# Kernel optimization log

Measured on AMD Instinct MI355X. Metric: run time of the kernel, lower is better.

The kernel has to match this reference:

```python
import jax, jax.numpy as jnp
import numpy as np

# dims: B batch, S src len, D input_size, H rnn hidden, E embedding_dim,
# V = output_size + 2 (vocab + Start/End), T = max target len (+2 for Start/End)
B, S, D, H, E, V, T = 128, 512, 256, 512, 256, 1002, 34
END = V - 1  # 'End' token index


def _gru_layer(x, h0, Wih, Whh, bih, bhh):
    """PyTorch-convention GRU layer. x: [B,T,Din], h0: [B,H].
    Wih: [3H,Din], Whh: [3H,H]. Returns (outputs [B,T,H], h_T [B,H])."""
    def step(h, xt):
        gi = xt @ Wih.T + bih            # [B,3H]
        gh = h @ Whh.T + bhh             # [B,3H]
        i_r, i_z, i_n = jnp.split(gi, 3, axis=-1)
        h_r, h_z, h_n = jnp.split(gh, 3, axis=-1)
        r = jax.nn.sigmoid(i_r + h_r)
        z = jax.nn.sigmoid(i_z + h_z)
        n = jnp.tanh(i_n + r * h_n)
        h_new = (1.0 - z) * n + z * h
        return h_new, h_new
    hT, ys = jax.lax.scan(step, h0, jnp.swapaxes(x, 0, 1))
    return jnp.swapaxes(ys, 0, 1), hT


def _gru_stack(x, h0s, layers):
    """h0s: [L,B,H]; layers: list of (Wih,Whh,bih,bhh). Returns (out, h [L,B,H])."""
    hs = []
    y = x
    for l, (Wih, Whh, bih, bhh) in enumerate(layers):
        y, hT = _gru_layer(y, h0s[l], Wih, Whh, bih, bhh)
        hs.append(hT)
    return y, jnp.stack(hs, axis=0)


def setup_inputs() -> dict:
    key = jax.random.key(0)
    ks = jax.random.split(key, 32)
    sc = 0.05
    inp = {}
    inp['source'] = jax.random.normal(ks[0], (B, S, D), dtype=jnp.float32)
    inp['target_ids'] = jax.random.randint(ks[1], (B, T), 0, V)
    inp['lengths'] = jax.random.randint(ks[2], (B,), 2, T + 1)
    inp['emb'] = sc * jax.random.normal(ks[3], (V, E), dtype=jnp.float32)
    # encoder layer 0 (in=D) and layer 1 (in=H)
    inp['enc_Wih0'] = sc * jax.random.normal(ks[4], (3 * H, D), dtype=jnp.float32)
    inp['enc_Whh0'] = sc * jax.random.normal(ks[5], (3 * H, H), dtype=jnp.float32)
    inp['enc_bih0'] = jnp.zeros((3 * H,), jnp.float32)
    inp['enc_bhh0'] = jnp.zeros((3 * H,), jnp.float32)
    inp['enc_Wih1'] = sc * jax.random.normal(ks[6], (3 * H, H), dtype=jnp.float32)
    inp['enc_Whh1'] = sc * jax.random.normal(ks[7], (3 * H, H), dtype=jnp.float32)
    inp['enc_bih1'] = jnp.zeros((3 * H,), jnp.float32)
    inp['enc_bhh1'] = jnp.zeros((3 * H,), jnp.float32)
    # decoder layer 0 (in=E) and layer 1 (in=H)
    inp['dec_Wih0'] = sc * jax.random.normal(ks[8], (3 * H, E), dtype=jnp.float32)
    inp['dec_Whh0'] = sc * jax.random.normal(ks[9], (3 * H, H), dtype=jnp.float32)
    inp['dec_bih0'] = jnp.zeros((3 * H,), jnp.float32)
    inp['dec_bhh0'] = jnp.zeros((3 * H,), jnp.float32)
    inp['dec_Wih1'] = sc * jax.random.normal(ks[10], (3 * H, H), dtype=jnp.float32)
    inp['dec_Whh1'] = sc * jax.random.normal(ks[11], (3 * H, H), dtype=jnp.float32)
    inp['dec_bih1'] = jnp.zeros((3 * H,), jnp.float32)
    inp['dec_bhh1'] = jnp.zeros((3 * H,), jnp.float32)
    # fc: H -> 5H -> 2H -> V
    inp['fc_W1'] = sc * jax.random.normal(ks[12], (5 * H, H), dtype=jnp.float32)
    inp['fc_b1'] = jnp.zeros((5 * H,), jnp.float32)
    inp['fc_W2'] = sc * jax.random.normal(ks[13], (2 * H, 5 * H), dtype=jnp.float32)
    inp['fc_b2'] = jnp.zeros((2 * H,), jnp.float32)
    inp['fc_W3'] = sc * jax.random.normal(ks[14], (V, 2 * H), dtype=jnp.float32)
    inp['fc_b3'] = jnp.zeros((V,), jnp.float32)
    return inp


def reference(source, target_ids, lengths, emb,
              enc_Wih0, enc_Whh0, enc_bih0, enc_bhh0,
              enc_Wih1, enc_Whh1, enc_bih1, enc_bhh1,
              dec_Wih0, dec_Whh0, dec_bih0, dec_bhh0,
              dec_Wih1, dec_Whh1, dec_bih1, dec_bhh1,
              fc_W1, fc_b1, fc_W2, fc_b2, fc_W3, fc_b3):
    Bx = source.shape[0]
    h0 = jnp.zeros((2, Bx, H), source.dtype)
    # encoder: only final hidden state h [L,B,H] is used
    _, h = _gru_stack(source, h0,
                      [(enc_Wih0, enc_Whh0, enc_bih0, enc_bhh0),
                       (enc_Wih1, enc_Whh1, enc_bih1, enc_bhh1)])
    # decoder over embedded (Start + target + End + pad) sequences
    tg = emb[target_ids]                               # [B,T,E]
    out, _ = _gru_stack(tg, h,
                        [(dec_Wih0, dec_Whh0, dec_bih0, dec_bhh0),
                         (dec_Wih1, dec_Whh1, dec_bih1, dec_bhh1)])
    # pad_packed_sequence zeroes timesteps >= length; sum over time
    mask = (jnp.arange(T)[None, :] < lengths[:, None]).astype(out.dtype)  # [B,T]
    pooled = jnp.einsum('bth,bt->bh', out, mask)       # [B,H]
    x = pooled @ fc_W1.T + fc_b1
    x = x @ fc_W2.T + fc_b2
    x = x @ fc_W3.T + fc_b3
    scores = jax.nn.sigmoid(x)                         # [B,V]
    # CrossEntropyLoss against the 'End' index for every row
    logp = jax.nn.log_softmax(scores, axis=-1)
    loss = -jnp.mean(logp[:, END])
    return loss
```

## Files before the change

### kernel.cpp

```cpp
#include <hip/hip_runtime.h>
#include <hip/hip_bf16.h>
#include <math.h>

#define B_ 128
#define S_ 512
#define D_ 256
#define H_ 512
#define E_ 256
#define V_ 1002
#define T_ 34
#define END_ 1001
#define NWG_TOTAL 128
#define BH (B_ * H_)
#define GPITCH 20

typedef __attribute__((ext_vector_type(8))) short short8;
typedef __attribute__((ext_vector_type(4))) float f32x4;
typedef __attribute__((ext_vector_type(4))) int i32x4;
typedef unsigned long long u64;

__device__ __forceinline__ float bf2f(unsigned short u){
  union { unsigned int i; float f; } x; x.i = ((unsigned int)u) << 16; return x.f;
}
__device__ __forceinline__ unsigned short f2bf(float f){
  union { float f; unsigned int i; } x; x.f = f;
  unsigned int r = x.i + 0x7fffu + ((x.i >> 16) & 1u);
  return (unsigned short)(r >> 16);
}
__device__ __forceinline__ float sigm(float x){ return 1.0f / (1.0f + expf(-x)); }

__device__ __forceinline__ void store_coh8(unsigned short* p, u64 v){
  __hip_atomic_store((u64*)p, v, __ATOMIC_RELAXED, __HIP_MEMORY_SCOPE_AGENT);
}

__device__ __forceinline__ i32x4 load_flags16(const unsigned* p){
  i32x4 r;
  asm volatile("global_load_dwordx4 %0, %1, off sc0 sc1\n\ts_waitcnt vmcnt(0)"
               : "=v"(r) : "v"(p) : "memory");
  return r;
}


__global__ void f2bf_kernel(const float* __restrict__ in, unsigned short* __restrict__ out, int n){
  int i = blockIdx.x * blockDim.x + threadIdx.x;
  int stride = gridDim.x * blockDim.x;
  for (; i < n; i += stride) out[i] = f2bf(in[i]);
}

__global__ void embed_kernel(const float* __restrict__ emb, const int* __restrict__ ids,
                             unsigned short* __restrict__ out){
  int i = blockIdx.x * blockDim.x + threadIdx.x;
  if (i >= B_ * T_ * E_) return;
  int bt = i >> 8;
  int e  = i & (E_ - 1);
  out[i] = f2bf(emb[(size_t)ids[bt] * E_ + e]);
}

__global__ void build_wcat(const float* __restrict__ Wih, const float* __restrict__ Whh,
                           unsigned short* __restrict__ Wcat, int Din){
  int K = Din + H_;
  int total = 2048 * K;
  int i = blockIdx.x * blockDim.x + threadIdx.x;
  int stride = gridDim.x * blockDim.x;
  for (; i < total; i += stride){
    int n = i / K, k = i - n * K;
    int g = n >> 9, j = n & 511;
    float v;
    if (g < 2){
      int r = (g << 9) + j;
      v = (k < Din) ? Wih[(size_t)r * Din + k] : Whh[(size_t)r * H_ + (k - Din)];
    } else if (g == 2){
      v = (k < Din) ? Wih[(size_t)(1024 + j) * Din + k] : 0.0f;
    } else {
      v = (k < Din) ? 0.0f : Whh[(size_t)(1024 + j) * H_ + (k - Din)];
    }
    Wcat[i] = f2bf(v);
  }
}

__global__ void build_bias(const float* __restrict__ bih, const float* __restrict__ bhh,
                           float* __restrict__ out){
  int j = blockIdx.x * blockDim.x + threadIdx.x;
  if (j >= 512) return;
  out[j]        = bih[j] + bhh[j];
  out[512 + j]  = bih[512 + j] + bhh[512 + j];
  out[1024 + j] = bih[1024 + j];
  out[1536 + j] = bhh[1024 + j];
}


template<int KT, int XKT>
__device__ __forceinline__ void run_layer(
    float* gbuf,
    const unsigned short* __restrict__ Wc, const float* __restrict__ bias4,
    const unsigned short* __restrict__ Xbase, int x_rs, int x_ts,
    const unsigned short* __restrict__ Hread,
    unsigned short* Hwrite,
    int T, unsigned round0,
    unsigned* own_flags, int slot,
    unsigned* prod_flags, unsigned prod0,
    u64* hprev,
    int jtile, int mh, int wv, int lane)
{
  constexpr int K   = KT * 32;
  constexpr int NSL = KT / 4;
  constexpr int XQ  = XKT / 4;
  constexpr int HQ  = NSL - XQ;
  const int tid  = threadIdx.x;
  const int ln   = lane & 15;
  const int lk8  = (lane >> 4) << 3;
  const int base_m = mh * 64;

  short8 wreg[4][NSL];
  #pragma unroll
  for (int g = 0; g < 4; ++g)
    #pragma unroll
    for (int j = 0; j < NSL; ++j)
      wreg[g][j] = *reinterpret_cast<const short8*>(
          Wc + (size_t)(g * 512 + jtile * 16 + ln) * K + (size_t)(wv + 4 * j) * 32 + lk8);

  const int erow  = tid >> 2;
  const int ecol0 = (tid & 3) << 2;
  const int ej    = (jtile << 4) + ecol0;
  const int egr   = base_m + erow;
  f32x4 bR, bZ, bNI, bNH;
  #pragma unroll
  for (int c = 0; c < 4; ++c){
    bR[c]  = bias4[ej + c];
    bZ[c]  = bias4[512 + ej + c];
    bNI[c] = bias4[1024 + ej + c];
    bNH[c] = bias4[1536 + ej + c];
  }

  const unsigned* pofs = own_flags + (lane & 7) * 4;
  const unsigned* ppfs = prod_flags ? (prod_flags + (lane & 7) * 4) : nullptr;

  for (int t = 0; t < T; ++t){
    const unsigned short* Xt  = Xbase + (size_t)t * x_ts;
    const unsigned short* Hin = Hread + (size_t)t * BH;

    if (ppfs){
      const unsigned prod_t = prod0 + (unsigned)t + 1u;
      for (;;){
        i32x4 g = load_flags16(ppfs);
        bool ok = (unsigned)g.x >= prod_t && (unsigned)g.y >= prod_t &&
                  (unsigned)g.z >= prod_t && (unsigned)g.w >= prod_t;
        if (__all(ok)) break;
        __builtin_amdgcn_s_sleep(1);
      }
      __builtin_amdgcn_sched_barrier(0);
    }

    i32x4 xf[XQ][4], hf[HQ][4];
    #pragma unroll
    for (int j = 0; j < XQ; ++j){
      const int kt = wv + 4 * j;
      #pragma unroll
      for (int mt = 0; mt < 4; ++mt){
        const unsigned short* p = Xt + (size_t)(base_m + mt * 16 + ln) * x_rs + kt * 32 + lk8;
        asm volatile("global_load_dwordx4 %0, %1, off" : "=v"(xf[j][mt]) : "v"(p));
      }
    }

    {
      const unsigned own_t = round0 + (unsigned)t;
      for (;;){
        i32x4 f = load_flags16(pofs);
        bool ok = (unsigned)f.x >= own_t && (unsigned)f.y >= own_t &&
                  (unsigned)f.z >= own_t && (unsigned)f.w >= own_t;
        if (__all(ok)) break;
        __builtin_amdgcn_s_sleep(1);
      }
      __builtin_amdgcn_sched_barrier(0);
    }

    #pragma unroll
    for (int j = 0; j < HQ; ++j){
      const int kt = wv + 4 * (XQ + j);
      #pragma unroll
      for (int mt = 0; mt < 4; ++mt){
        const unsigned short* p = Hin + (size_t)(base_m + mt * 16 + ln) * H_ + (kt - XKT) * 32 + lk8;
        asm volatile("global_load_dwordx4 %0, %1, off" : "=v"(hf[j][mt]) : "v"(p));
      }
    }
    __builtin_amdgcn_sched_barrier(0);

    f32x4 acc[4][4];
    #pragma unroll
    for (int g = 0; g < 4; ++g)
      #pragma unroll
      for (int mt = 0; mt < 4; ++mt) acc[g][mt] = (f32x4){0.f, 0.f, 0.f, 0.f};

    #pragma unroll
    for (int j = 0; j < XQ; ++j)
      #pragma unroll
      for (int g = 0; g < 4; ++g)
        #pragma unroll
        for (int mt = 0; mt < 4; ++mt)
          acc[g][mt] = __builtin_amdgcn_mfma_f32_16x16x32_bf16(
              __builtin_bit_cast(short8, xf[j][mt]), wreg[g][j], acc[g][mt], 0, 0, 0);

    asm volatile("s_waitcnt vmcnt(0)" ::: "memory");
    __builtin_amdgcn_sched_barrier(0);
    #pragma unroll
    for (int j = 0; j < HQ; ++j)
      #pragma unroll
      for (int g = 0; g < 4; ++g)
        #pragma unroll
        for (int mt = 0; mt < 4; ++mt)
          acc[g][mt] = __builtin_amdgcn_mfma_f32_16x16x32_bf16(
              __builtin_bit_cast(short8, hf[j][mt]), wreg[g][XQ + j], acc[g][mt], 0, 0, 0);

    #pragma unroll
    for (int g = 0; g < 4; ++g)
      #pragma unroll
      for (int mt = 0; mt < 4; ++mt){
        const int rl = mt * 16 + ((lane >> 4) << 2);
        #pragma unroll
        for (int i = 0; i < 4; ++i)
          gbuf[((wv * 4 + g) * 64 + rl + i) * GPITCH + ln] = acc[g][mt][i];
      }
    __syncthreads();

    {
      f32x4 p0 = (f32x4){0.f,0.f,0.f,0.f}, p1 = p0, p2 = p0, p3 = p0;
      #pragma unroll
      for (int qq = 0; qq < 4; ++qq){
        p0 += *reinterpret_cast<const f32x4*>(gbuf + ((qq * 4 + 0) * 64 + erow) * GPITCH + ecol0);
        p1 += *reinterpret_cast<const f32x4*>(gbuf + ((qq * 4 + 1) * 64 + erow) * GPITCH + ecol0);
        p2 += *reinterpret_cast<const f32x4*>(gbuf + ((qq * 4 + 2) * 64 + erow) * GPITCH + ecol0);
        p3 += *reinterpret_cast<const f32x4*>(gbuf + ((qq * 4 + 3) * 64 + erow) * GPITCH + ecol0);
      }
      u64 hv = *hprev;
      u64 hb = 0;
      #pragma unroll
      for (int c = 0; c < 4; ++c){
        float rr = sigm(p0[c] + bR[c]);
        float zz = sigm(p1[c] + bZ[c]);
        float nn = tanhf(p2[c] + bNI[c] + rr * (p3[c] + bNH[c]));
        float hp = bf2f((unsigned short)(hv >> (16 * c)));
        float hn = (1.0f - zz) * nn + zz * hp;
        hb |= ((u64)f2bf(hn)) << (16 * c);
      }
      *hprev = hb;
      store_coh8(Hwrite + (size_t)t * BH + ((size_t)egr << 9) + ej, hb);
    }

    asm volatile("s_waitcnt vmcnt(0)" ::: "memory");
    __syncthreads();
    if (tid == 0)
      __hip_atomic_store(own_flags + slot, round0 + (unsigned)t + 1u,
                         __ATOMIC_RELAXED, __HIP_MEMORY_SCOPE_AGENT);
  }
}

__global__ __launch_bounds__(256, 1)
void rnn_persistent(
    const unsigned short* __restrict__ src, const unsigned short* __restrict__ tg,
    const unsigned short* __restrict__ Wc_e0, const unsigned short* __restrict__ Wc_e1,
    const unsigned short* __restrict__ Wc_d0, const unsigned short* __restrict__ Wc_d1,
    const float* __restrict__ b_e0, const float* __restrict__ b_e1,
    const float* __restrict__ b_d0, const float* __restrict__ b_d1,
    unsigned short* H0, unsigned short* H1,
    unsigned* flags)
{
  __shared__ __align__(16) float gbuf[16 * 64 * GPITCH];
  __builtin_amdgcn_fence(__ATOMIC_ACQUIRE, "agent");
  const int wg = blockIdx.x;
  const int layer = wg >> 6;
  const int gidx = wg & 63;
  const int jtile = gidx & 31, mh = gidx >> 5;
  const int wv = threadIdx.x >> 6, lane = threadIdx.x & 63;
  unsigned* own  = flags + (size_t)((layer << 1) | mh) * 64;
  unsigned* prod = flags + (size_t)mh * 64;
  u64 hprev = 0;
  if (layer == 0){
    run_layer<24, 8>(gbuf, Wc_e0, b_e0, src, S_ * D_, D_,
                     H0, H0 + BH, S_, 0u, own, jtile, nullptr, 0u, &hprev,
                     jtile, mh, wv, lane);
    run_layer<24, 8>(gbuf, Wc_d0, b_d0, tg, T_ * E_, E_,
                     H0 + (size_t)512 * BH, H0 + (size_t)513 * BH, T_, 512u,
                     own, jtile, nullptr, 0u, &hprev,
                     jtile, mh, wv, lane);
  } else {
    run_layer<32, 16>(gbuf, Wc_e1, b_e1, H0 + BH, H_, BH,
                      H1, H1 + BH, S_, 0u, own, jtile, prod, 0u, &hprev,
                      jtile, mh, wv, lane);
    run_layer<32, 16>(gbuf, Wc_d1, b_d1, H0 + (size_t)513 * BH, H_, BH,
                      H1 + (size_t)512 * BH, H1 + (size_t)513 * BH, T_, 512u,
                      own, jtile, prod, 512u, &hprev,
                      jtile, mh, wv, lane);
  }
}

__global__ __launch_bounds__(256)
void gemm_nt(const unsigned short* __restrict__ A, const unsigned short* __restrict__ W,
             const float* __restrict__ bias,
             unsigned short* __restrict__ outB, float* __restrict__ outF,
             int M, int N, int K, int act)
{
  const int w    = threadIdx.x >> 6;
  const int lane = threadIdx.x & 63;
  const int ln   = lane & 15;
  const int lk8  = (lane >> 4) << 3;
  const int row0 = blockIdx.y * 32;
  const int col0 = blockIdx.x * 256 + w * 64;

  f32x4 acc[2][4];
  #pragma unroll
  for (int a = 0; a < 2; a++)
    #pragma unroll
    for (int g = 0; g < 4; g++) acc[a][g] = (f32x4){0.f, 0.f, 0.f, 0.f};

  const unsigned short* arow0 = A + (size_t)(row0 + ln) * K;
  const unsigned short* arow1 = A + (size_t)(row0 + 16 + ln) * K;
  const unsigned short* wrow[4];
  int ncol[4];
  #pragma unroll
  for (int nt = 0; nt < 4; ++nt){
    int n = col0 + nt * 16 + ln;
    ncol[nt] = n;
    int nc = n < N ? n : (N - 1);
    wrow[nt] = W + (size_t)nc * K;
  }

  const int nk = K >> 5;
  for (int kt = 0; kt < nk; ++kt){
    const int k = (kt << 5) + lk8;
    short8 a0 = *reinterpret_cast<const short8*>(arow0 + k);
    short8 a1 = *reinterpret_cast<const short8*>(arow1 + k);
    #pragma unroll
    for (int nt = 0; nt < 4; ++nt){
      short8 bf = *reinterpret_cast<const short8*>(wrow[nt] + k);
      acc[0][nt] = __builtin_amdgcn_mfma_f32_16x16x32_bf16(a0, bf, acc[0][nt], 0, 0, 0);
      acc[1][nt] = __builtin_amdgcn_mfma_f32_16x16x32_bf16(a1, bf, acc[1][nt], 0, 0, 0);
    }
  }

  #pragma unroll
  for (int nt = 0; nt < 4; ++nt){
    const int n = ncol[nt];
    if (n >= N) continue;
    const float bv = bias ? bias[n] : 0.0f;
    #pragma unroll
    for (int mt = 0; mt < 2; ++mt){
      const int rbase = row0 + mt * 16 + ((lane >> 4) << 2);
      #pragma unroll
      for (int reg = 0; reg < 4; ++reg){
        const int row = rbase + reg;
        if (row >= M) continue;
        float v = acc[mt][nt][reg] + bv;
        if (act == 1) v = sigm(v);
        if (outB) outB[(size_t)row * N + n] = f2bf(v);
        if (outF) outF[(size_t)row * N + n] = v;
      }
    }
  }
}


__global__ void pool_kernel(const unsigned short* __restrict__ H1, const int* __restrict__ lengths,
                            unsigned short* __restrict__ pooled){
  int i = blockIdx.x * blockDim.x + threadIdx.x;
  if (i >= B_ * H_) return;
  int b = i >> 9;
  int j = i & (H_ - 1);
  int len = lengths[b]; if (len > T_) len = T_;
  float s = 0.0f;
  for (int t = 0; t < len; ++t)
    s += bf2f(H1[(size_t)(513 + t) * BH + ((size_t)b << 9) + j]);
  pooled[i] = f2bf(s);
}

__global__ void loss_kernel(const float* __restrict__ scores, float* __restrict__ out){
  __shared__ float wsum[4];
  const int w = threadIdx.x >> 6;
  const int lane = threadIdx.x & 63;
  float acc = 0.0f;
  for (int b = w; b < B_; b += 4){
    const float* row = scores + (size_t)b * V_;
    float vals[16];
    float mx = -1e30f;
    #pragma unroll
    for (int i = 0; i < 16; ++i){
      int c = lane + i * 64;
      vals[i] = (c < V_) ? row[c] : -1e30f;
      mx = fmaxf(mx, vals[i]);
    }
    #pragma unroll
    for (int off = 32; off; off >>= 1) mx = fmaxf(mx, __shfl_xor(mx, off));
    float se = 0.0f;
    #pragma unroll
    for (int i = 0; i < 16; ++i){
      int c = lane + i * 64;
      if (c < V_) se += expf(vals[i] - mx);
    }
    #pragma unroll
    for (int off = 32; off; off >>= 1) se += __shfl_xor(se, off);
    float logp = row[END_] - (mx + logf(se));
    acc += logp;
  }
  if (lane == 0) wsum[w] = acc;
  __syncthreads();
  if (threadIdx.x == 0){
    out[0] = -(wsum[0] + wsum[1] + wsum[2] + wsum[3]) / (float)B_;
  }
}


extern "C" void kernel_launch(void* const* d_in, const int* in_sizes, int n_in,
                              void* d_out, int out_size, void* d_ws, size_t ws_size,
                              hipStream_t stream) {
  const float* source   = (const float*)d_in[0];
  const int*   tgt_ids  = (const int*)  d_in[1];
  const int*   lengths  = (const int*)  d_in[2];
  const float* emb      = (const float*)d_in[3];
  const float* eWih0 = (const float*)d_in[4],  *eWhh0 = (const float*)d_in[5];
  const float* ebih0 = (const float*)d_in[6],  *ebhh0 = (const float*)d_in[7];
  const float* eWih1 = (const float*)d_in[8],  *eWhh1 = (const float*)d_in[9];
  const float* ebih1 = (const float*)d_in[10], *ebhh1 = (const float*)d_in[11];
  const float* dWih0 = (const float*)d_in[12], *dWhh0 = (const float*)d_in[13];
  const float* dbih0 = (const float*)d_in[14], *dbhh0 = (const float*)d_in[15];
  const float* dWih1 = (const float*)d_in[16], *dWhh1 = (const float*)d_in[17];
  const float* dbih1 = (const float*)d_in[18], *dbhh1 = (const float*)d_in[19];
  const float* fcW1 = (const float*)d_in[20], *fcb1 = (const float*)d_in[21];
  const float* fcW2 = (const float*)d_in[22], *fcb2 = (const float*)d_in[23];
  const float* fcW3 = (const float*)d_in[24], *fcb3 = (const float*)d_in[25];

  char* p = (char*)d_ws;
  auto alloc = [&](size_t bytes) -> void* {
    void* r = (void*)p;
    p += (bytes + 255) & ~(size_t)255;
    return r;
  };

  unsigned short* src_bf = (unsigned short*)alloc((size_t)B_ * S_ * D_ * 2);
  unsigned short* tg_bf  = (unsigned short*)alloc((size_t)B_ * T_ * E_ * 2);
  unsigned short* H0 = (unsigned short*)alloc((size_t)547 * BH * 2);
  unsigned short* H1 = (unsigned short*)alloc((size_t)547 * BH * 2);
  unsigned short* Wc_e0 = (unsigned short*)alloc((size_t)2048 * 768  * 2);
  unsigned short* Wc_e1 = (unsigned short*)alloc((size_t)2048 * 1024 * 2);
  unsigned short* Wc_d0 = (unsigned short*)alloc((size_t)2048 * 768  * 2);
  unsigned short* Wc_d1 = (unsigned short*)alloc((size_t)2048 * 1024 * 2);
  float* bias_e0 = (float*)alloc(2048 * 4);
  float* bias_e1 = (float*)alloc(2048 * 4);
  float* bias_d0 = (float*)alloc(2048 * 4);
  float* bias_d1 = (float*)alloc(2048 * 4);
  unsigned short* fcW1b = (unsigned short*)alloc((size_t)2560 * 512  * 2);
  unsigned short* fcW2b = (unsigned short*)alloc((size_t)1024 * 2560 * 2);
  unsigned short* fcW3b = (unsigned short*)alloc((size_t)V_ * 1024 * 2);
  unsigned short* pooled = (unsigned short*)alloc((size_t)B_ * H_ * 2);
  unsigned short* x1_bf  = (unsigned short*)alloc((size_t)B_ * 2560 * 2);
  unsigned short* x2_bf  = (unsigned short*)alloc((size_t)B_ * 1024 * 2);
  float* scores = (float*)alloc((size_t)B_ * V_ * 4);
  unsigned* flags = (unsigned*)alloc(4 * 64 * 4);

  f2bf_kernel<<<8192, 256, 0, stream>>>(source, src_bf, B_ * S_ * D_);
  embed_kernel<<<(B_ * T_ * E_ + 255) / 256, 256, 0, stream>>>(emb, tgt_ids, tg_bf);
  build_wcat<<<2048, 256, 0, stream>>>(eWih0, eWhh0, Wc_e0, D_);
  build_wcat<<<2048, 256, 0, stream>>>(eWih1, eWhh1, Wc_e1, H_);
  build_wcat<<<2048, 256, 0, stream>>>(dWih0, dWhh0, Wc_d0, E_);
  build_wcat<<<2048, 256, 0, stream>>>(dWih1, dWhh1, Wc_d1, H_);
  build_bias<<<2, 256, 0, stream>>>(ebih0, ebhh0, bias_e0);
  build_bias<<<2, 256, 0, stream>>>(ebih1, ebhh1, bias_e1);
  build_bias<<<2, 256, 0, stream>>>(dbih0, dbhh0, bias_d0);
  build_bias<<<2, 256, 0, stream>>>(dbih1, dbhh1, bias_d1);
  f2bf_kernel<<<4096, 256, 0, stream>>>(fcW1, fcW1b, 2560 * 512);
  f2bf_kernel<<<4096, 256, 0, stream>>>(fcW2, fcW2b, 1024 * 2560);
  f2bf_kernel<<<4096, 256, 0, stream>>>(fcW3, fcW3b, V_ * 1024);

  hipMemsetAsync(H0, 0, (size_t)BH * 2, stream);
  hipMemsetAsync(H1, 0, (size_t)BH * 2, stream);
  hipMemsetAsync(flags, 0, 4 * 64 * 4, stream);

  rnn_persistent<<<NWG_TOTAL, 256, 0, stream>>>(
      src_bf, tg_bf, Wc_e0, Wc_e1, Wc_d0, Wc_d1,
      bias_e0, bias_e1, bias_d0, bias_d1,
      H0, H1, flags);

  pool_kernel<<<(B_ * H_ + 255) / 256, 256, 0, stream>>>(H1, lengths, pooled);

  {
    dim3 g1((2560 + 255) / 256, B_ / 32);
    gemm_nt<<<g1, 256, 0, stream>>>(pooled, fcW1b, fcb1, x1_bf, (float*)nullptr,
                                    B_, 2560, 512, 0);
    dim3 g2((1024 + 255) / 256, B_ / 32);
    gemm_nt<<<g2, 256, 0, stream>>>(x1_bf, fcW2b, fcb2, x2_bf, (float*)nullptr,
                                    B_, 1024, 2560, 0);
    dim3 g3((V_ + 255) / 256, B_ / 32);
    gemm_nt<<<g3, 256, 0, stream>>>(x2_bf, fcW3b, fcb3, (unsigned short*)nullptr, scores,
                                    B_, V_, 1024, 1);
  }

  loss_kernel<<<1, 256, 0, stream>>>(scores, (float*)d_out);
}
```

Measured before the change: 4.154 ms.

## Use per-wave completion flags, XCD-aware workgroup mapping, and dual-scope hidden-state stores

The persistent GRU kernel now launches 256 workgroups and keeps only those with (blockIdx & 7) < 4. Under round-robin dispatch this puts each layer and half-batch role on a fixed subset of XCDs, so producers and consumers share an L2. Each wave publishes its own completion flag after its stores drain, replacing the block-wide barrier plus single flag. Consumers poll 32x4 flags per group. Hidden-state stores go out twice, once as a normal store (local L2) and once with sc0 sc1 (coherent), so same-XCD readers may hit cache. The risks are reliance on an undocumented dispatch order, more flag polling, and extra store traffic.

```diff
diff --git a/kernel.cpp b/kernel.cpp
--- a/kernel.cpp
+++ b/kernel.cpp
@@ -10,7 +10,7 @@
 #define V_ 1002
 #define T_ 34
 #define END_ 1001
-#define NWG_TOTAL 128
+#define NWG_LAUNCH 256
 #define BH (B_ * H_)
 #define GPITCH 20
 
@@ -29,8 +29,9 @@
 }
 __device__ __forceinline__ float sigm(float x){ return 1.0f / (1.0f + expf(-x)); }
 
-__device__ __forceinline__ void store_coh8(unsigned short* p, u64 v){
-  __hip_atomic_store((u64*)p, v, __ATOMIC_RELAXED, __HIP_MEMORY_SCOPE_AGENT);
+__device__ __forceinline__ void store_dual8(unsigned short* p, u64 v){
+  asm volatile("global_store_dwordx2 %0, %1, off"         :: "v"(p), "v"(v) : "memory");
+  asm volatile("global_store_dwordx2 %0, %1, off sc0 sc1" :: "v"(p), "v"(v) : "memory");
 }
 
 __device__ __forceinline__ i32x4 load_flags16(const unsigned* p){
@@ -97,7 +98,7 @@
     const unsigned short* __restrict__ Hread,
     unsigned short* Hwrite,
     int T, unsigned round0,
-    unsigned* own_flags, int slot,
+    unsigned* own_flags,
     unsigned* prod_flags, unsigned prod0,
     u64* hprev,
     int jtile, int mh, int wv, int lane)
@@ -132,8 +133,9 @@
     bNH[c] = bias4[1536 + ej + c];
   }
 
-  const unsigned* pofs = own_flags + (lane & 7) * 4;
-  const unsigned* ppfs = prod_flags ? (prod_flags + (lane & 7) * 4) : nullptr;
+  const unsigned* pofs = own_flags + (lane & 31) * 4;
+  const unsigned* ppfs = prod_flags ? (prod_flags + (lane & 31) * 4) : nullptr;
+  const int myslot = jtile * 4 + wv;
 
   for (int t = 0; t < T; ++t){
     const unsigned short* Xt  = Xbase + (size_t)t * x_ts;
@@ -211,6 +213,8 @@
           acc[g][mt] = __builtin_amdgcn_mfma_f32_16x16x32_bf16(
               __builtin_bit_cast(short8, hf[j][mt]), wreg[g][XQ + j], acc[g][mt], 0, 0, 0);
 
+    __syncthreads();
+
     #pragma unroll
     for (int g = 0; g < 4; ++g)
       #pragma unroll
@@ -243,13 +247,12 @@
         hb |= ((u64)f2bf(hn)) << (16 * c);
       }
       *hprev = hb;
-      store_coh8(Hwrite + (size_t)t * BH + ((size_t)egr << 9) + ej, hb);
+      store_dual8(Hwrite + (size_t)t * BH + ((size_t)egr << 9) + ej, hb);
     }
 
     asm volatile("s_waitcnt vmcnt(0)" ::: "memory");
-    __syncthreads();
-    if (tid == 0)
-      __hip_atomic_store(own_flags + slot, round0 + (unsigned)t + 1u,
+    if (lane == 0)
+      __hip_atomic_store(own_flags + myslot, round0 + (unsigned)t + 1u,
                          __ATOMIC_RELAXED, __HIP_MEMORY_SCOPE_AGENT);
   }
 }
@@ -265,30 +268,32 @@
     unsigned* flags)
 {
   __shared__ __align__(16) float gbuf[16 * 64 * GPITCH];
+  const int wg = blockIdx.x;
+  const int hint = wg & 7;
+  if (hint >= 4) return;
   __builtin_amdgcn_fence(__ATOMIC_ACQUIRE, "agent");
-  const int wg = blockIdx.x;
-  const int layer = wg >> 6;
-  const int gidx = wg & 63;
-  const int jtile = gidx & 31, mh = gidx >> 5;
+  const int layer = hint >> 1;
+  const int mh    = hint & 1;
+  const int jtile = wg >> 3;
   const int wv = threadIdx.x >> 6, lane = threadIdx.x & 63;
-  unsigned* own  = flags + (size_t)((layer << 1) | mh) * 64;
-  unsigned* prod = flags + (size_t)mh * 64;
+  unsigned* own  = flags + (size_t)((layer << 1) | mh) * 128;
+  unsigned* prod = flags + (size_t)mh * 128;
   u64 hprev = 0;
   if (layer == 0){
     run_layer<24, 8>(gbuf, Wc_e0, b_e0, src, S_ * D_, D_,
-                     H0, H0 + BH, S_, 0u, own, jtile, nullptr, 0u, &hprev,
+                     H0, H0 + BH, S_, 0u, own, nullptr, 0u, &hprev,
                      jtile, mh, wv, lane);
     run_layer<24, 8>(gbuf, Wc_d0, b_d0, tg, T_ * E_, E_,
                      H0 + (size_t)512 * BH, H0 + (size_t)513 * BH, T_, 512u,
-                     own, jtile, nullptr, 0u, &hprev,
+                     own, nullptr, 0u, &hprev,
                      jtile, mh, wv, lane);
   } else {
     run_layer<32, 16>(gbuf, Wc_e1, b_e1, H0 + BH, H_, BH,
-                      H1, H1 + BH, S_, 0u, own, jtile, prod, 0u, &hprev,
+                      H1, H1 + BH, S_, 0u, own, prod, 0u, &hprev,
                       jtile, mh, wv, lane);
     run_layer<32, 16>(gbuf, Wc_d1, b_d1, H0 + (size_t)513 * BH, H_, BH,
                       H1 + (size_t)512 * BH, H1 + (size_t)513 * BH, T_, 512u,
-                      own, jtile, prod, 512u, &hprev,
+                      own, prod, 512u, &hprev,
                       jtile, mh, wv, lane);
   }
 }
@@ -453,7 +458,7 @@
   unsigned short* x1_bf  = (unsigned short*)alloc((size_t)B_ * 2560 * 2);
   unsigned short* x2_bf  = (unsigned short*)alloc((size_t)B_ * 1024 * 2);
   float* scores = (float*)alloc((size_t)B_ * V_ * 4);
-  unsigned* flags = (unsigned*)alloc(4 * 64 * 4);
+  unsigned* flags = (unsigned*)alloc(4 * 128 * 4);
 
   f2bf_kernel<<<8192, 256, 0, stream>>>(source, src_bf, B_ * S_ * D_);
   embed_kernel<<<(B_ * T_ * E_ + 255) / 256, 256, 0, stream>>>(emb, tgt_ids, tg_bf);
@@ -471,9 +476,9 @@
 
   hipMemsetAsync(H0, 0, (size_t)BH * 2, stream);
   hipMemsetAsync(H1, 0, (size_t)BH * 2, stream);
-  hipMemsetAsync(flags, 0, 4 * 64 * 4, stream);
-
-  rnn_persistent<<<NWG_TOTAL, 256, 0, stream>>>(
+  hipMemsetAsync(flags, 0, 4 * 128 * 4, stream);
+
+  rnn_persistent<<<NWG_LAUNCH, 256, 0, stream>>>(
       src_bf, tg_bf, Wc_e0, Wc_e1, Wc_d0, Wc_d1,
       bias_e0, bias_e1, bias_d0, bias_d1,
       H0, H1, flags);
```

After: 6.697 ms. +61.2%, slower.
